# Performance work log

Measured on AMD Instinct MI355X. Metric: run time of the kernel, lower is better.

## Reference

```python
import jax, jax.numpy as jnp
import numpy as np

D_MODEL = 512
NUM_HEADS = 8
HEAD_DIM = D_MODEL // NUM_HEADS


def setup_inputs() -> dict:
    key = jax.random.key(0)
    ks = jax.random.split(key, 9)
    B, N, D = 2, 4096, D_MODEL
    scale = 1.0 / np.sqrt(D)
    inp = {
        "x": jax.random.normal(ks[0], (B, N, D), dtype=jnp.float32),
        "wq": jax.random.normal(ks[1], (D, D), dtype=jnp.float32) * scale,
        "bq": jnp.zeros((D,), dtype=jnp.float32),
        "wk": jax.random.normal(ks[2], (D, D), dtype=jnp.float32) * scale,
        "bk": jnp.zeros((D,), dtype=jnp.float32),
        "wv": jax.random.normal(ks[3], (D, D), dtype=jnp.float32) * scale,
        "bv": jnp.zeros((D,), dtype=jnp.float32),
        "wo": jax.random.normal(ks[4], (D, D), dtype=jnp.float32) * scale,
        "bo": jnp.zeros((D,), dtype=jnp.float32),
    }
    return inp


def reference(x, wq, bq, wk, bk, wv, bv, wo, bo):
    B, N, D = x.shape
    h, dh = NUM_HEADS, HEAD_DIM
    # QKV projections (torch Linear: x @ W.T + b); reshape to [B, h, N, dh]
    def proj(w, b):
        y = jnp.einsum('bnd,ed->bne', x, w) + b
        return y.reshape(B, N, h, dh).transpose(0, 2, 1, 3)
    q = proj(wq, bq)
    k = proj(wk, bk)
    v = proj(wv, bv)
    # scaled dot-product attention, full [B, h, N, N] scores (matches module)
    attn = jnp.einsum('bhqd,bhkd->bhqk', q, k) / jnp.sqrt(jnp.float32(dh)).astype(x.dtype)
    attn = jax.nn.softmax(attn, axis=-1)
    y = jnp.einsum('bhqk,bhkd->bhqd', attn, v)
    y = y.transpose(0, 2, 1, 3).reshape(B, N, D)
    # output projection
    return jnp.einsum('bnd,ed->bne', y, wo) + bo
```

## Files before the change

### kernel.cpp

```cpp
#include <hip/hip_runtime.h>
#include <hip/hip_bf16.h>

#define NN 4096
#define DD 512
#define HH 8
#define DH 64
#define BN 8192
#define PAIRS 16

typedef unsigned int uint32;
typedef __attribute__((ext_vector_type(8))) short short8;
typedef __attribute__((ext_vector_type(4))) float f32x4;

__device__ __forceinline__ float blo(uint32 u) {
    union { uint32 i; float f; } c; c.i = u << 16; return c.f;
}
__device__ __forceinline__ unsigned short f2b(float x) {
    union { float f; uint32 u; } c; c.f = x;
    return (unsigned short)((c.u + 0x8000u) >> 16);
}
__device__ __forceinline__ uint32 pack2(float lo, float hi) {
    return (uint32)f2b(lo) | ((uint32)f2b(hi) << 16);
}
__device__ __forceinline__ uint32 cvtpk(float lo, float hi) {
    uint32 r;
    asm("v_cvt_pk_bf16_f32 %0, %1, %2" : "=v"(r) : "v"(lo), "v"(hi));
    return r;
}
__device__ __forceinline__ float expsc(float s) {
    return __builtin_amdgcn_exp2f(fminf(s, 86.5f));
}
#define QSCALE 0.18033688011112042f

__global__ void detect_dtype(const uint32* __restrict__ xw, uint32* __restrict__ flag) {
    __shared__ int cnt;
    if (threadIdx.x == 0) cnt = 0;
    __syncthreads();
    int c = 0;
    for (int i = threadIdx.x; i < 1024; i += 64) {
        uint32 e = (xw[i] >> 7) & 0xFFu;
        if (e >= 110u && e <= 135u) c++;
    }
    atomicAdd(&cnt, c);
    __syncthreads();
    if (threadIdx.x == 0) *flag = (cnt < 512) ? 1u : 0u;
}

__global__ __launch_bounds__(256) void conv_x(const void* __restrict__ src,
                                              unsigned short* __restrict__ dst,
                                              const uint32* __restrict__ flagp) {
    int i0 = (blockIdx.x * 256 + threadIdx.x) * 8;
    if (*flagp) {
        const float4* s = (const float4*)src;
        float4 a = s[i0 >> 2], b = s[(i0 >> 2) + 1];
        uint4 o;
        o.x = pack2(a.x, a.y); o.y = pack2(a.z, a.w);
        o.z = pack2(b.x, b.y); o.w = pack2(b.z, b.w);
        *(uint4*)(dst + i0) = o;
    } else {
        *(uint4*)(dst + i0) = ((const uint4*)src)[i0 >> 3];
    }
}

__global__ __launch_bounds__(256) void conv_w(const void* s0, const void* s1,
                                              const void* s2, const void* s3,
                                              unsigned short* __restrict__ dst,
                                              const uint32* __restrict__ flagp) {
    int seg = blockIdx.x >> 7;
    const void* src = (seg == 0) ? s0 : (seg == 1) ? s1 : (seg == 2) ? s2 : s3;
    unsigned short* d = dst + (size_t)seg * DD * DD;
    int i0 = ((blockIdx.x & 127) * 256 + threadIdx.x) * 8;
    if (*flagp) {
        const float4* s = (const float4*)src;
        float4 a = s[i0 >> 2], b = s[(i0 >> 2) + 1];
        uint4 o;
        o.x = pack2(a.x, a.y); o.y = pack2(a.z, a.w);
        o.z = pack2(b.x, b.y); o.w = pack2(b.z, b.w);
        *(uint4*)(d + i0) = o;
    } else {
        *(uint4*)(d + i0) = ((const uint4*)src)[i0 >> 3];
    }
}

__global__ __launch_bounds__(256) void conv_b(const void* s0, const void* s1,
                                              const void* s2, const void* s3,
                                              float* __restrict__ dst,
                                              const uint32* __restrict__ flagp) {
    const void* sl[4] = { s0, s1, s2, s3 };
    int fp32mode = (int)*flagp;
    #pragma unroll
    for (int m = 0; m < 4; ++m) {
        #pragma unroll
        for (int j = 0; j < 2; ++j) {
            int i = threadIdx.x * 2 + j;
            float v;
            if (fp32mode) v = ((const float*)sl[m])[i];
            else {
                union { uint32 u; float f; } c;
                c.u = ((uint32)((const unsigned short*)sl[m])[i]) << 16;
                v = c.f;
            }
            dst[m * DD + i] = v;
        }
    }
}

__global__ __launch_bounds__(256) void qkv_gemm(
    const unsigned short* __restrict__ xb,
    const unsigned short* __restrict__ wsb,
    const float* __restrict__ bsf,
    unsigned short* __restrict__ Qb, unsigned short* __restrict__ Kb,
    unsigned short* __restrict__ VTg)
{
    __shared__ unsigned short As[128 * 40];
    __shared__ unsigned short Bs[128 * 40];
    const int tid = threadIdx.x;
    const int mat = blockIdx.x >> 8;
    const int rem = blockIdx.x & 255;
    const int nt = rem >> 6, mt = rem & 63;
    const int m0 = mt * 128, n0 = nt * 128;
    const int w = tid >> 6, lane = tid & 63, quad = lane >> 4, col = lane & 15;
    const int wr = w >> 1, wc = w & 1;
    const unsigned short* wm = wsb + (size_t)mat * DD * DD;
    const bool qk = (mat < 2);

    f32x4 acc[4][4];
    #pragma unroll
    for (int i = 0; i < 4; ++i)
        #pragma unroll
        for (int j = 0; j < 4; ++j)
            acc[i][j] = (f32x4){0.f, 0.f, 0.f, 0.f};

    for (int kt = 0; kt < 16; ++kt) {
        int k0 = kt * 32;
        __syncthreads();
        #pragma unroll
        for (int it = 0; it < 2; ++it) {
            int idx = tid + it * 256;
            int row = idx >> 2, c4 = idx & 3;
            *(uint4*)&As[row * 40 + c4 * 8] =
                *(const uint4*)(xb + (size_t)(m0 + row) * DD + k0 + c4 * 8);
            *(uint4*)&Bs[row * 40 + c4 * 8] =
                *(const uint4*)(wm + (size_t)(n0 + row) * DD + k0 + c4 * 8);
        }
        __syncthreads();
        if (qk) {
            short8 wf[4], xf[4];
            #pragma unroll
            for (int i = 0; i < 4; ++i)
                wf[i] = *(const short8*)&Bs[(wr * 64 + i * 16 + col) * 40 + quad * 8];
            #pragma unroll
            for (int j = 0; j < 4; ++j)
                xf[j] = *(const short8*)&As[(wc * 64 + j * 16 + col) * 40 + quad * 8];
            #pragma unroll
            for (int i = 0; i < 4; ++i)
                #pragma unroll
                for (int j = 0; j < 4; ++j)
                    acc[i][j] = __builtin_amdgcn_mfma_f32_16x16x32_bf16(
                        wf[i], xf[j], acc[i][j], 0, 0, 0);
        } else {
            short8 xf[4], wf[4];
            #pragma unroll
            for (int i = 0; i < 4; ++i)
                xf[i] = *(const short8*)&As[(wr * 64 + i * 16 + col) * 40 + quad * 8];
            #pragma unroll
            for (int j = 0; j < 4; ++j)
                wf[j] = *(const short8*)&Bs[(wc * 64 + j * 16 + col) * 40 + quad * 8];
            #pragma unroll
            for (int i = 0; i < 4; ++i)
                #pragma unroll
                for (int j = 0; j < 4; ++j)
                    acc[i][j] = __builtin_amdgcn_mfma_f32_16x16x32_bf16(
                        xf[i], wf[j], acc[i][j], 0, 0, 0);
        }
    }

    if (qk) {
        unsigned short* Om = (mat == 0) ? Qb : Kb;
        const float qs = (mat == 0) ? QSCALE : 1.0f;
        #pragma unroll
        for (int i = 0; i < 4; ++i) {
            int e0 = n0 + wr * 64 + i * 16 + quad * 4;
            float4 bj = *(const float4*)(bsf + mat * DD + e0);
            int h = e0 >> 6, jj0 = e0 & 63;
            #pragma unroll
            for (int j = 0; j < 4; ++j) {
                int g = m0 + wc * 64 + j * 16 + col;
                int b = g >> 12, n = g & (NN - 1);
                uint32 lo = pack2((acc[i][j][0] + bj.x) * qs, (acc[i][j][1] + bj.y) * qs);
                uint32 hi = pack2((acc[i][j][2] + bj.z) * qs, (acc[i][j][3] + bj.w) * qs);
                uint2 v; v.x = lo; v.y = hi;
                *(uint2*)(Om + ((size_t)((b << 3) + h) * NN + n) * DH + jj0) = v;
            }
        }
    } else {
        #pragma unroll
        for (int j = 0; j < 4; ++j) {
            int e = n0 + wc * 64 + j * 16 + col;
            float bj = bsf[2 * DD + e];
            int h = e >> 6, jj = e & 63;
            #pragma unroll
            for (int i = 0; i < 4; ++i) {
                int g0 = m0 + wr * 64 + i * 16 + quad * 4;
                int b = g0 >> 12, n = g0 & (NN - 1);
                uint32 lo = pack2(acc[i][j][0] + bj, acc[i][j][1] + bj);
                uint32 hi = pack2(acc[i][j][2] + bj, acc[i][j][3] + bj);
                uint2 v; v.x = lo; v.y = hi;
                *(uint2*)(VTg + ((size_t)((b << 3) + h) * DH + jj) * NN + n) = v;
            }
        }
    }
}

__global__ __launch_bounds__(512, 4) void attn_mfma(
    const unsigned short* __restrict__ Qb,
    const unsigned short* __restrict__ Kb,
    const unsigned short* __restrict__ VTg,
    unsigned short* __restrict__ Ob)
{
    __shared__ unsigned short Kt[2][64 * 72];
    __shared__ unsigned short Vt[2][64 * 72];
    __shared__ unsigned short Pt[128 * 72];

    const int tid  = threadIdx.x;
    const int w    = tid >> 6;
    const int lane = tid & 63;
    const int quad = lane >> 4;
    const int col  = lane & 15;
    const int pair = blockIdx.x >> 5;
    const int chunk = blockIdx.x & 31;
    const size_t base = (size_t)pair * NN;
    const int n0 = chunk * 128;
    const int qbase = w * 16;

    short8 qf[2];
    #pragma unroll
    for (int kk = 0; kk < 2; ++kk)
        qf[kk] = *(const short8*)(Qb +
            (base + n0 + qbase + col) * DH + kk * 32 + quad * 8);

    f32x4 accO[4];
    #pragma unroll
    for (int tc = 0; tc < 4; ++tc) accO[tc] = (f32x4){0.f, 0.f, 0.f, 0.f};
    float lsum = 0.f;

    const int skey = tid >> 3;
    const int sc8  = (tid & 7) * 8;
    const unsigned short* Kg = Kb + base * DH;
    const unsigned short* Vg = VTg + (size_t)pair * DH * NN;
    const int prow = (qbase + col) * 72;

    uint4 kreg = *(const uint4*)(Kg + (size_t)skey * DH + sc8);
    uint4 vreg = *(const uint4*)(Vg + (size_t)skey * NN + sc8);
    *(uint4*)&Kt[0][skey * 72 + sc8] = kreg;
    *(uint4*)&Vt[0][skey * 72 + sc8] = vreg;
    kreg = *(const uint4*)(Kg + (size_t)(64 + skey) * DH + sc8);
    vreg = *(const uint4*)(Vg + (size_t)skey * NN + 64 + sc8);
    __syncthreads();

    for (int kt = 0; kt < NN / 64; ++kt) {
        const int buf = kt & 1;
        if (kt + 1 < NN / 64) {
            *(uint4*)&Kt[buf ^ 1][skey * 72 + sc8] = kreg;
            *(uint4*)&Vt[buf ^ 1][skey * 72 + sc8] = vreg;
            int tn = (kt + 2 < NN / 64) ? kt + 2 : 0;
            kreg = *(const uint4*)(Kg + (size_t)(tn * 64 + skey) * DH + sc8);
            vreg = *(const uint4*)(Vg + (size_t)skey * NN + tn * 64 + sc8);
        }
        const unsigned short* Kc = &Kt[buf][0];
        const unsigned short* Vc = &Vt[buf][0];

        f32x4 s[4];
        #pragma unroll
        for (int tc = 0; tc < 4; ++tc) s[tc] = (f32x4){0.f, 0.f, 0.f, 0.f};
        __builtin_amdgcn_s_setprio(1);
        #pragma unroll
        for (int tc = 0; tc < 4; ++tc) {
            #pragma unroll
            for (int kk = 0; kk < 2; ++kk) {
                short8 kf = *(const short8*)&Kc[(tc * 16 + col) * 72 + kk * 32 + quad * 8];
                s[tc] = __builtin_amdgcn_mfma_f32_16x16x32_bf16(kf, qf[kk], s[tc], 0, 0, 0);
            }
        }
        __builtin_amdgcn_s_setprio(0);

        #pragma unroll
        for (int tc = 0; tc < 4; ++tc) {
            float p0 = expsc(s[tc][0]);
            float p1 = expsc(s[tc][1]);
            float p2 = expsc(s[tc][2]);
            float p3 = expsc(s[tc][3]);
            lsum += (p0 + p1) + (p2 + p3);
            uint2 v; v.x = cvtpk(p0, p1); v.y = cvtpk(p2, p3);
            *(uint2*)&Pt[prow + tc * 16 + quad * 4] = v;
        }

        short8 pf[2];
        #pragma unroll
        for (int ks = 0; ks < 2; ++ks)
            pf[ks] = *(const short8*)&Pt[prow + ks * 32 + quad * 8];

        __builtin_amdgcn_s_setprio(1);
        #pragma unroll
        for (int tc = 0; tc < 4; ++tc) {
            short8 vf0 = *(const short8*)&Vc[(tc * 16 + col) * 72 + quad * 8];
            short8 vf1 = *(const short8*)&Vc[(tc * 16 + col) * 72 + 32 + quad * 8];
            accO[tc] = __builtin_amdgcn_mfma_f32_16x16x32_bf16(pf[0], vf0, accO[tc], 0, 0, 0);
            accO[tc] = __builtin_amdgcn_mfma_f32_16x16x32_bf16(pf[1], vf1, accO[tc], 0, 0, 0);
        }
        __builtin_amdgcn_s_setprio(0);

        __syncthreads();
    }

    lsum += __shfl_xor(lsum, 16);
    lsum += __shfl_xor(lsum, 32);

    float inv[4];
    #pragma unroll
    for (int r = 0; r < 4; ++r)
        inv[r] = 1.f / __shfl(lsum, quad * 4 + r);

    #pragma unroll
    for (int tc = 0; tc < 4; ++tc)
        #pragma unroll
        for (int r = 0; r < 4; ++r) {
            float v = accO[tc][r] * inv[r];
            Ob[(base + n0 + qbase + quad * 4 + r) * DH + tc * 16 + col] = f2b(v);
        }
}

__global__ __launch_bounds__(256) void out_gemm(
    const unsigned short* __restrict__ Ob,
    const unsigned short* __restrict__ wob,
    const float* __restrict__ bof,
    const uint32* __restrict__ flagp,
    void* __restrict__ outp)
{
    __shared__ unsigned short As[128 * 40];
    __shared__ unsigned short Bs[128 * 40];
    const int tid = threadIdx.x;
    const int nt = blockIdx.x >> 6, mt = blockIdx.x & 63;
    const int m0 = mt * 128, n0 = nt * 128;
    const int w = tid >> 6, lane = tid & 63, quad = lane >> 4, col = lane & 15;
    const int wr = w >> 1, wc = w & 1;
    const int fp32mode = (int)*flagp;

    f32x4 acc[4][4];
    #pragma unroll
    for (int i = 0; i < 4; ++i)
        #pragma unroll
        for (int j = 0; j < 4; ++j)
            acc[i][j] = (f32x4){0.f, 0.f, 0.f, 0.f};

    for (int kt = 0; kt < 16; ++kt) {
        int k0 = kt * 32;
        int h = k0 >> 6, koff = k0 & 63;
        __syncthreads();
        #pragma unroll
        for (int it = 0; it < 2; ++it) {
            int idx = tid + it * 256;
            int row = idx >> 2, c4 = idx & 3;
            int g = m0 + row, b = g >> 12, n = g & (NN - 1);
            *(uint4*)&As[row * 40 + c4 * 8] = *(const uint4*)(Ob +
                ((size_t)((b << 3) + h) * NN + n) * DH + koff + c4 * 8);
            *(uint4*)&Bs[row * 40 + c4 * 8] =
                *(const uint4*)(wob + (size_t)(n0 + row) * DD + k0 + c4 * 8);
        }
        __syncthreads();
        short8 wf[4], yf[4];
        #pragma unroll
        for (int i = 0; i < 4; ++i)
            wf[i] = *(const short8*)&Bs[(wr * 64 + i * 16 + col) * 40 + quad * 8];
        #pragma unroll
        for (int j = 0; j < 4; ++j)
            yf[j] = *(const short8*)&As[(wc * 64 + j * 16 + col) * 40 + quad * 8];
        #pragma unroll
        for (int i = 0; i < 4; ++i)
            #pragma unroll
            for (int j = 0; j < 4; ++j)
                acc[i][j] = __builtin_amdgcn_mfma_f32_16x16x32_bf16(
                    wf[i], yf[j], acc[i][j], 0, 0, 0);
    }

    #pragma unroll
    for (int i = 0; i < 4; ++i) {
        int e0 = n0 + wr * 64 + i * 16 + quad * 4;
        float4 bj = *(const float4*)(bof + e0);
        #pragma unroll
        for (int j = 0; j < 4; ++j) {
            int g = m0 + wc * 64 + j * 16 + col;
            float v0 = acc[i][j][0] + bj.x;
            float v1 = acc[i][j][1] + bj.y;
            float v2 = acc[i][j][2] + bj.z;
            float v3 = acc[i][j][3] + bj.w;
            if (fp32mode) {
                float4 o; o.x = v0; o.y = v1; o.z = v2; o.w = v3;
                *(float4*)((float*)outp + (size_t)g * DD + e0) = o;
            } else {
                uint2 o; o.x = pack2(v0, v1); o.y = pack2(v2, v3);
                *(uint2*)((unsigned short*)outp + (size_t)g * DD + e0) = o;
            }
        }
    }
}

extern "C" void kernel_launch(void* const* d_in, const int* in_sizes, int n_in,
                              void* d_out, int out_size, void* d_ws, size_t ws_size,
                              hipStream_t stream) {
    char* p = (char*)d_ws;
    uint32* flag = (uint32*)p;                  p += 256;
    unsigned short* xb  = (unsigned short*)p;   p += (size_t)BN * DD * 2;
    unsigned short* wsb = (unsigned short*)p;   p += (size_t)4 * DD * DD * 2;
    float*          bsf = (float*)p;            p += (size_t)4 * DD * 4;
    unsigned short* Qb  = (unsigned short*)p;   p += (size_t)PAIRS * NN * DH * 2;
    unsigned short* Kb  = (unsigned short*)p;   p += (size_t)PAIRS * NN * DH * 2;
    unsigned short* VTg = (unsigned short*)p;   p += (size_t)PAIRS * NN * DH * 2;
    unsigned short* Ob  = (unsigned short*)p;   p += (size_t)PAIRS * NN * DH * 2;

    detect_dtype<<<1, 64, 0, stream>>>((const uint32*)d_in[0], flag);
    conv_x<<<BN * DD / 2048, 256, 0, stream>>>(d_in[0], xb, flag);
    conv_w<<<512, 256, 0, stream>>>(d_in[1], d_in[3], d_in[5], d_in[7], wsb, flag);
    conv_b<<<1, 256, 0, stream>>>(d_in[2], d_in[4], d_in[6], d_in[8], bsf, flag);
    qkv_gemm<<<768, 256, 0, stream>>>(xb, wsb, bsf, Qb, Kb, VTg);
    attn_mfma<<<PAIRS * 32, 512, 0, stream>>>(Qb, Kb, VTg, Ob);
    out_gemm<<<256, 256, 0, stream>>>(Ob, wsb + (size_t)3 * DD * DD,
                                      bsf + 3 * DD, flag, d_out);
}
```

Baseline: 249.5 us.

## Keep softmax P in registers via permlane swaps and shrink attention blocks

The attention kernel no longer stages the exponentiated score tile P through shared memory. The MFMA output is instead rearranged into the A-operand layout with v_permlane32/16_swap instructions, which removes LDS writes and reads from every key-tile iteration. Blocks shrink from 512 to 256 threads (64 queries each) and the grid doubles, so each thread now loads two 16-byte chunks per K/V tile. This halves K/V tile reuse per block and doubles global K/V traffic, in exchange for less shared memory and more blocks in flight.

```diff
diff --git a/kernel.cpp b/kernel.cpp
--- a/kernel.cpp
+++ b/kernel.cpp
@@ -212,7 +212,7 @@
     }
 }
 
-__global__ __launch_bounds__(512, 4) void attn_mfma(
+__global__ __launch_bounds__(256, 4) void attn_mfma(
     const unsigned short* __restrict__ Qb,
     const unsigned short* __restrict__ Kb,
     const unsigned short* __restrict__ VTg,
@@ -220,17 +220,16 @@
 {
     __shared__ unsigned short Kt[2][64 * 72];
     __shared__ unsigned short Vt[2][64 * 72];
-    __shared__ unsigned short Pt[128 * 72];
 
     const int tid  = threadIdx.x;
     const int w    = tid >> 6;
     const int lane = tid & 63;
     const int quad = lane >> 4;
     const int col  = lane & 15;
-    const int pair = blockIdx.x >> 5;
-    const int chunk = blockIdx.x & 31;
+    const int pair = blockIdx.x >> 6;
+    const int chunk = blockIdx.x & 63;
     const size_t base = (size_t)pair * NN;
-    const int n0 = chunk * 128;
+    const int n0 = chunk * 64;
     const int qbase = w * 16;
 
     short8 qf[2];
@@ -244,61 +243,79 @@
     for (int tc = 0; tc < 4; ++tc) accO[tc] = (f32x4){0.f, 0.f, 0.f, 0.f};
     float lsum = 0.f;
 
-    const int skey = tid >> 3;
-    const int sc8  = (tid & 7) * 8;
+    const int srow = tid >> 2;
+    const int sce  = (tid & 3) * 16;
     const unsigned short* Kg = Kb + base * DH;
     const unsigned short* Vg = VTg + (size_t)pair * DH * NN;
-    const int prow = (qbase + col) * 72;
-
-    uint4 kreg = *(const uint4*)(Kg + (size_t)skey * DH + sc8);
-    uint4 vreg = *(const uint4*)(Vg + (size_t)skey * NN + sc8);
-    *(uint4*)&Kt[0][skey * 72 + sc8] = kreg;
-    *(uint4*)&Vt[0][skey * 72 + sc8] = vreg;
-    kreg = *(const uint4*)(Kg + (size_t)(64 + skey) * DH + sc8);
-    vreg = *(const uint4*)(Vg + (size_t)skey * NN + 64 + sc8);
+
+    uint4 kreg[2], vreg[2];
+    #pragma unroll
+    for (int r = 0; r < 2; ++r) {
+        kreg[r] = *(const uint4*)(Kg + (size_t)srow * DH + sce + r * 8);
+        vreg[r] = *(const uint4*)(Vg + (size_t)srow * NN + sce + r * 8);
+    }
+    #pragma unroll
+    for (int r = 0; r < 2; ++r) {
+        *(uint4*)&Kt[0][srow * 72 + sce + r * 8] = kreg[r];
+        *(uint4*)&Vt[0][srow * 72 + sce + r * 8] = vreg[r];
+    }
+    #pragma unroll
+    for (int r = 0; r < 2; ++r) {
+        kreg[r] = *(const uint4*)(Kg + (size_t)(64 + srow) * DH + sce + r * 8);
+        vreg[r] = *(const uint4*)(Vg + (size_t)srow * NN + 64 + sce + r * 8);
+    }
     __syncthreads();
 
     for (int kt = 0; kt < NN / 64; ++kt) {
         const int buf = kt & 1;
         if (kt + 1 < NN / 64) {
-            *(uint4*)&Kt[buf ^ 1][skey * 72 + sc8] = kreg;
-            *(uint4*)&Vt[buf ^ 1][skey * 72 + sc8] = vreg;
+            #pragma unroll
+            for (int r = 0; r < 2; ++r) {
+                *(uint4*)&Kt[buf ^ 1][srow * 72 + sce + r * 8] = kreg[r];
+                *(uint4*)&Vt[buf ^ 1][srow * 72 + sce + r * 8] = vreg[r];
+            }
             int tn = (kt + 2 < NN / 64) ? kt + 2 : 0;
-            kreg = *(const uint4*)(Kg + (size_t)(tn * 64 + skey) * DH + sc8);
-            vreg = *(const uint4*)(Vg + (size_t)skey * NN + tn * 64 + sc8);
+            #pragma unroll
+            for (int r = 0; r < 2; ++r) {
+                kreg[r] = *(const uint4*)(Kg + (size_t)(tn * 64 + srow) * DH + sce + r * 8);
+                vreg[r] = *(const uint4*)(Vg + (size_t)srow * NN + tn * 64 + sce + r * 8);
+            }
         }
         const unsigned short* Kc = &Kt[buf][0];
         const unsigned short* Vc = &Vt[buf][0];
 
-        f32x4 s[4];
-        #pragma unroll
-        for (int tc = 0; tc < 4; ++tc) s[tc] = (f32x4){0.f, 0.f, 0.f, 0.f};
-        __builtin_amdgcn_s_setprio(1);
-        #pragma unroll
-        for (int tc = 0; tc < 4; ++tc) {
+        short8 pf[2];
+        #pragma unroll
+        for (int half = 0; half < 2; ++half) {
+            f32x4 s0 = (f32x4){0.f, 0.f, 0.f, 0.f};
+            f32x4 s1 = (f32x4){0.f, 0.f, 0.f, 0.f};
+            __builtin_amdgcn_s_setprio(1);
             #pragma unroll
             for (int kk = 0; kk < 2; ++kk) {
-                short8 kf = *(const short8*)&Kc[(tc * 16 + col) * 72 + kk * 32 + quad * 8];
-                s[tc] = __builtin_amdgcn_mfma_f32_16x16x32_bf16(kf, qf[kk], s[tc], 0, 0, 0);
-            }
-        }
-        __builtin_amdgcn_s_setprio(0);
-
-        #pragma unroll
-        for (int tc = 0; tc < 4; ++tc) {
-            float p0 = expsc(s[tc][0]);
-            float p1 = expsc(s[tc][1]);
-            float p2 = expsc(s[tc][2]);
-            float p3 = expsc(s[tc][3]);
-            lsum += (p0 + p1) + (p2 + p3);
-            uint2 v; v.x = cvtpk(p0, p1); v.y = cvtpk(p2, p3);
-            *(uint2*)&Pt[prow + tc * 16 + quad * 4] = v;
-        }
-
-        short8 pf[2];
-        #pragma unroll
-        for (int ks = 0; ks < 2; ++ks)
-            pf[ks] = *(const short8*)&Pt[prow + ks * 32 + quad * 8];
+                short8 kf0 = *(const short8*)&Kc[((half * 2 + 0) * 16 + col) * 72 + kk * 32 + quad * 8];
+                short8 kf1 = *(const short8*)&Kc[((half * 2 + 1) * 16 + col) * 72 + kk * 32 + quad * 8];
+                s0 = __builtin_amdgcn_mfma_f32_16x16x32_bf16(kf0, qf[kk], s0, 0, 0, 0);
+                s1 = __builtin_amdgcn_mfma_f32_16x16x32_bf16(kf1, qf[kk], s1, 0, 0, 0);
+            }
+            __builtin_amdgcn_s_setprio(0);
+
+            float p00 = expsc(s0[0]), p01 = expsc(s0[1]);
+            float p02 = expsc(s0[2]), p03 = expsc(s0[3]);
+            float p10 = expsc(s1[0]), p11 = expsc(s1[1]);
+            float p12 = expsc(s1[2]), p13 = expsc(s1[3]);
+            lsum += ((p00 + p01) + (p02 + p03)) + ((p10 + p11) + (p12 + p13));
+            uint32 a0 = cvtpk(p00, p01);
+            uint32 a1 = cvtpk(p02, p03);
+            uint32 b0 = cvtpk(p10, p11);
+            uint32 b1 = cvtpk(p12, p13);
+            asm("v_permlane32_swap_b32 %0, %1" : "+v"(a0), "+v"(b0));
+            asm("v_permlane32_swap_b32 %0, %1" : "+v"(a1), "+v"(b1));
+            asm("v_permlane16_swap_b32 %0, %1" : "+v"(a0), "+v"(b0));
+            asm("v_permlane16_swap_b32 %0, %1" : "+v"(a1), "+v"(b1));
+            union { uint32 u[4]; short8 v; } pu;
+            pu.u[0] = a0; pu.u[1] = a1; pu.u[2] = b0; pu.u[3] = b1;
+            pf[half] = pu.v;
+        }
 
         __builtin_amdgcn_s_setprio(1);
         #pragma unroll
@@ -423,7 +440,7 @@
     conv_w<<<512, 256, 0, stream>>>(d_in[1], d_in[3], d_in[5], d_in[7], wsb, flag);
     conv_b<<<1, 256, 0, stream>>>(d_in[2], d_in[4], d_in[6], d_in[8], bsf, flag);
     qkv_gemm<<<768, 256, 0, stream>>>(xb, wsb, bsf, Qb, Kb, VTg);
-    attn_mfma<<<PAIRS * 32, 512, 0, stream>>>(Qb, Kb, VTg, Ob);
+    attn_mfma<<<PAIRS * 64, 256, 0, stream>>>(Qb, Kb, VTg, Ob);
     out_gemm<<<256, 256, 0, stream>>>(Ob, wsb + (size_t)3 * DD * DD,
                                       bsf + 3 * DD, flag, d_out);
 }
```

New measurement: 422.6 us. +69.4%, slower.
